# Kernel tuning notes

Hardware: AMD Instinct MI355X
Metric: run time of the kernel (lower is better)

The kernel has to match this reference:

```python
import jax, jax.numpy as jnp
import numpy as np

NUM_USERS = 1024
NUM_BUSINESSES = 2048
N_NODES = NUM_USERS + NUM_BUSINESSES  # 3072
B = 1024            # batch size (== NUM_USERS to keep the business_idx-offset bug valid)
E = 16384           # edges (self loops added inside reference, PyG GATConv default)
H = 768             # hidden_size
HEADS = 8
NUM_IMAGES = 3


def setup_inputs() -> dict:
    key = jax.random.key(0)
    ks = jax.random.split(key, 24)
    def rn(k, shape, s=0.02):
        return jax.random.normal(k, shape, dtype=jnp.float32) * s
    inp = {
        'text_cls': rn(ks[0], (B, 768), 1.0),              # BERT CLS features
        'img_cls': rn(ks[1], (B, NUM_IMAGES, 768), 1.0),   # ViT CLS features per image
        'biz_feats': rn(ks[2], (B, 3), 1.0),
        'W_text': rn(ks[3], (768, H)), 'b_text': jnp.zeros((H,), jnp.float32),
        'W_img': rn(ks[4], (768, H)), 'b_img': jnp.zeros((H,), jnp.float32),
        'W_bf': rn(ks[5], (3, H)), 'b_bf': jnp.zeros((H,), jnp.float32),
        'user_table': rn(ks[6], (NUM_USERS, H)),
        'biz_table': rn(ks[7], (NUM_BUSINESSES, H)),
        'W1': rn(ks[8], (H, HEADS * H)),
        'att_src1': rn(ks[9], (HEADS, H), 0.1),
        'att_dst1': rn(ks[10], (HEADS, H), 0.1),
        'b1': jnp.zeros((HEADS * H,), jnp.float32),
        'W2': rn(ks[11], (HEADS * H, H)),
        'att_src2': rn(ks[12], (1, H), 0.1),
        'att_dst2': rn(ks[13], (1, H), 0.1),
        'b2': jnp.zeros((H,), jnp.float32),
        'Wf1': rn(ks[14], (4 * H, 2 * H)), 'bf1': jnp.zeros((2 * H,), jnp.float32),
        'Wf2': rn(ks[15], (2 * H, H)), 'bf2': jnp.zeros((H,), jnp.float32),
        'Wf3': rn(ks[16], (H, 1)), 'bf3': jnp.zeros((1,), jnp.float32),
        'user_idx': jax.random.randint(ks[17], (B,), 0, NUM_USERS),
        'business_idx': jax.random.randint(ks[18], (B,), NUM_USERS, N_NODES),
        'edge_index': jax.random.randint(ks[19], (2, E), 0, N_NODES),
    }
    return inp


def gat_conv(x, src, dst, W, a_src, a_dst, bias, heads):
    # PyG GATConv: linear -> per-head additive attention -> scatter softmax over dst -> scatter add
    N = x.shape[0]
    C = W.shape[1] // heads
    h = (x @ W).reshape(N, heads, C)                       # [N,H,C]
    s_src = jnp.sum(h * a_src, axis=-1)                    # [N,H]
    s_dst = jnp.sum(h * a_dst, axis=-1)                    # [N,H]
    e = jax.nn.leaky_relu(s_src[src] + s_dst[dst], 0.2)    # [E,H]
    e_max = jax.ops.segment_max(e, dst, num_segments=N)    # [N,H]
    ee = jnp.exp(e - e_max[dst])
    denom = jax.ops.segment_sum(ee, dst, num_segments=N)   # [N,H]
    alpha = ee / (denom[dst] + 1e-16)                      # [E,H]
    out = jax.ops.segment_sum(h[src] * alpha[..., None], dst, num_segments=N)  # [N,H,C]
    return out.reshape(N, heads * C) + bias


def reference(text_cls, img_cls, biz_feats, W_text, b_text, W_img, b_img, W_bf, b_bf,
              user_table, biz_table, W1, att_src1, att_dst1, b1, W2, att_src2, att_dst2, b2,
              Wf1, bf1, Wf2, bf2, Wf3, bf3, user_idx, business_idx, edge_index):
    text_emb = text_cls @ W_text + b_text                       # TextEncoder.fc
    img_emb = jnp.mean(img_cls, axis=1) @ W_img + b_img         # ImageEncoder mean + fc
    meta = biz_feats @ W_bf + b_bf                              # business_feature_fc
    user_emb = user_table[user_idx]
    biz_emb = biz_table[business_idx - user_idx.shape[0]]       # faithful: offset by batch size
    x = jnp.zeros((N_NODES, H), jnp.float32)
    x = x.at[user_idx].set(user_emb)
    x = x.at[business_idx].set((text_emb + img_emb + meta + biz_emb) / 4.0)
    loop = jnp.arange(N_NODES)
    src = jnp.concatenate([edge_index[0], loop])                # add self loops (PyG default)
    dst = jnp.concatenate([edge_index[1], loop])
    x = jax.nn.relu(gat_conv(x, src, dst, W1, att_src1, att_dst1, b1, HEADS))
    x = gat_conv(x, src, dst, W2, att_src2, att_dst2, b2, 1)
    cat = jnp.concatenate([x[user_idx], x[business_idx], text_emb, img_emb], axis=1)  # [B,4H]
    h1 = jax.nn.relu(cat @ Wf1 + bf1)
    h2 = jax.nn.relu(h1 @ Wf2 + bf2)
    return (h2 @ Wf3 + bf3).squeeze(-1)                         # [B]
```

## Files before the change

kernel.cpp:

```cpp
#include <hip/hip_runtime.h>
#include <hip/hip_bf16.h>

namespace {

constexpr int kB = 1024;
constexpr int kNU = 1024;
constexpr int kNB = 2048;
constexpr int kNN = 3072;
constexpr int kE = 16384;
constexpr int kET = kE + kNN;
constexpr int kH = 768;
constexpr int kHeads = 8;
constexpr int kSplitK = 4;

typedef __attribute__((ext_vector_type(8))) short bf16x8_t;
typedef __attribute__((ext_vector_type(4))) float f32x4_t;

__device__ __forceinline__ float tof(float x) { return x; }
__device__ __forceinline__ float tof(__hip_bfloat16 x) { return __bfloat162float(x); }
__device__ __forceinline__ void stor(float* p, float v) { *p = v; }
__device__ __forceinline__ void stor(__hip_bfloat16* p, float v) { *p = __float2bfloat16(v); }

__device__ __forceinline__ float blo(unsigned u) {
  union { unsigned u; float f; } c; c.u = u << 16; return c.f;
}
__device__ __forceinline__ float bhi(unsigned u) {
  union { unsigned u; float f; } c; c.u = u & 0xffff0000u; return c.f;
}

__device__ __forceinline__ unsigned pk2(float a, float b) {
  union { __hip_bfloat16 h[2]; unsigned u; } c;
  c.h[0] = __float2bfloat16(a); c.h[1] = __float2bfloat16(b);
  return c.u;
}

__device__ __forceinline__ void gload_lds16(const void* g, void* l) {
  __builtin_amdgcn_global_load_lds(
      (const __attribute__((address_space(1))) void*)g,
      (__attribute__((address_space(3))) void*)l, 16, 0, 0);
}

template <int BM, int BN, int FM, int FN, typename TC>
__device__ __forceinline__ void gemm_body(
    const __hip_bfloat16* __restrict__ A, const __hip_bfloat16* __restrict__ Bt,
    const float* __restrict__ bias, TC* __restrict__ C,
    int K, int lda, int ldc, int act, int bx, int by) {
  __shared__ __align__(16) __hip_bfloat16 As[2][BM][32];
  __shared__ __align__(16) __hip_bfloat16 Bs[2][BN][32];
  const int t = threadIdx.x;
  const int w = t >> 6, lane = t & 63;
  const int wm = w >> 1, wn = w & 1;
  const int bm = by * BM, bn = bx * BN;
  const int lr = lane & 15, lg = lane >> 4;

  f32x4_t acc[FM][FN];
#pragma unroll
  for (int m = 0; m < FM; ++m)
#pragma unroll
    for (int n = 0; n < FN; ++n) acc[m][n] = (f32x4_t){0.f, 0.f, 0.f, 0.f};

  auto stage = [&](int buf, int kt) {
    const int k0 = kt << 5;
#pragma unroll
    for (int i = 0; i < BM / 64; ++i) {
      int L = i * 256 + t;
      gload_lds16(A + (size_t)(bm + (L >> 2)) * lda + k0 + (L & 3) * 8,
                  (char*)(&As[buf][0][0]) + ((size_t)(i * 256 + w * 64)) * 16);
    }
#pragma unroll
    for (int i = 0; i < BN / 64; ++i) {
      int L = i * 256 + t;
      gload_lds16(Bt + (size_t)(bn + (L >> 2)) * K + k0 + (L & 3) * 8,
                  (char*)(&Bs[buf][0][0]) + ((size_t)(i * 256 + w * 64)) * 16);
    }
  };

  const int NT = K >> 5;
  stage(0, 0);
  __syncthreads();
  for (int kt = 0; kt < NT; ++kt) {
    const int cur = kt & 1;
    if (kt + 1 < NT) stage(cur ^ 1, kt + 1);
    bf16x8_t af[FM], bv[FN];
#pragma unroll
    for (int m = 0; m < FM; ++m)
      af[m] = *(const bf16x8_t*)&As[cur][wm * FM * 16 + m * 16 + lr][lg * 8];
#pragma unroll
    for (int n = 0; n < FN; ++n)
      bv[n] = *(const bf16x8_t*)&Bs[cur][wn * FN * 16 + n * 16 + lr][lg * 8];
#pragma unroll
    for (int m = 0; m < FM; ++m)
#pragma unroll
      for (int n = 0; n < FN; ++n)
        acc[m][n] = __builtin_amdgcn_mfma_f32_16x16x32_bf16(af[m], bv[n], acc[m][n], 0, 0, 0);
    __syncthreads();
  }

#pragma unroll
  for (int m = 0; m < FM; ++m) {
    const int row0 = bm + wm * FM * 16 + m * 16 + lg * 4;
#pragma unroll
    for (int n = 0; n < FN; ++n) {
      const int cn = bn + wn * FN * 16 + n * 16 + lr;
      const float bvv = bias ? bias[cn] : 0.f;
#pragma unroll
      for (int r = 0; r < 4; ++r) {
        float v = acc[m][n][r] + bvv;
        if (act) v = fmaxf(v, 0.f);
        stor(&C[(size_t)(row0 + r) * ldc + cn], v);
      }
    }
  }
}

__device__ __forceinline__ void swz_xy(bool mfast, int& bx, int& by) {
  const int nwg = gridDim.x * gridDim.y;
  const int orig = blockIdx.y * gridDim.x + blockIdx.x;
  const int swz = (orig & 7) * (nwg >> 3) + (orig >> 3);
  if (mfast) { by = swz % gridDim.y; bx = swz / gridDim.y; }
  else       { bx = swz % gridDim.x; by = swz / gridDim.x; }
}

template <int BM, int BN, int FM, int FN, typename TC, bool MFAST>
__global__ __launch_bounds__(256) void mfma_gemm(
    const __hip_bfloat16* __restrict__ A, const __hip_bfloat16* __restrict__ Bt,
    const float* __restrict__ bias, TC* __restrict__ C,
    int N, int K, int act) {
  int bx, by;
  swz_xy(MFAST, bx, by);
  gemm_body<BM, BN, FM, FN, TC>(A, Bt, bias, C, K, K, N, act, bx, by);
}

template <int BM, int BN, int FM, int FN>
__global__ __launch_bounds__(256) void mfma_gemm_dual(
    const __hip_bfloat16* __restrict__ A0, const __hip_bfloat16* __restrict__ Bt0,
    const float* __restrict__ bias0, float* __restrict__ C0,
    const __hip_bfloat16* __restrict__ A1, const __hip_bfloat16* __restrict__ Bt1,
    const float* __restrict__ bias1, float* __restrict__ C1,
    int N, int K) {
  int bx, by;
  swz_xy(true, bx, by);
  const __hip_bfloat16* A = blockIdx.z ? A1 : A0;
  const __hip_bfloat16* Bt = blockIdx.z ? Bt1 : Bt0;
  const float* bias = blockIdx.z ? bias1 : bias0;
  float* C = blockIdx.z ? C1 : C0;
  gemm_body<BM, BN, FM, FN, float>(A, Bt, bias, C, K, K, N, 0, bx, by);
}

template <int BM, int BN, int FM, int FN>
__global__ __launch_bounds__(256) void gemm_head(
    const __hip_bfloat16* __restrict__ y, const __hip_bfloat16* __restrict__ W1t,
    const float* __restrict__ b1, __hip_bfloat16* __restrict__ x2) {
  const int hd = blockIdx.x;
  const int tile = blockIdx.y;
  const int bx = tile % (kH / BN);
  const int by = tile / (kH / BN);
  gemm_body<BM, BN, FM, FN, __hip_bfloat16>(
      y + (size_t)hd * kH, W1t + (size_t)hd * kH * kH, b1 + hd * kH,
      x2 + (size_t)hd * kH, kH, kHeads * kH, kHeads * kH, 1, bx, by);
}

template <int BM, int BN, int FM, int FN>
__global__ __launch_bounds__(256) void mfma_gemm_splitk(
    const __hip_bfloat16* __restrict__ A, const __hip_bfloat16* __restrict__ Bt,
    float* __restrict__ Cpart, int M, int N, int K, int KC) {
  __shared__ __align__(16) __hip_bfloat16 As[2][BM][32];
  __shared__ __align__(16) __hip_bfloat16 Bs[2][BN][32];
  int bx, by;
  swz_xy(false, bx, by);
  const int t = threadIdx.x;
  const int w = t >> 6, lane = t & 63;
  const int wm = w >> 1, wn = w & 1;
  const int bm = by * BM, bn = bx * BN;
  const int kbeg = blockIdx.z * KC;
  const int lr = lane & 15, lg = lane >> 4;

  f32x4_t acc[FM][FN];
#pragma unroll
  for (int m = 0; m < FM; ++m)
#pragma unroll
    for (int n = 0; n < FN; ++n) acc[m][n] = (f32x4_t){0.f, 0.f, 0.f, 0.f};

  auto stage = [&](int buf, int kt) {
    const int k0 = kbeg + (kt << 5);
#pragma unroll
    for (int i = 0; i < BM / 64; ++i) {
      int L = i * 256 + t;
      gload_lds16(A + (size_t)(bm + (L >> 2)) * K + k0 + (L & 3) * 8,
                  (char*)(&As[buf][0][0]) + ((size_t)(i * 256 + w * 64)) * 16);
    }
#pragma unroll
    for (int i = 0; i < BN / 64; ++i) {
      int L = i * 256 + t;
      gload_lds16(Bt + (size_t)(bn + (L >> 2)) * K + k0 + (L & 3) * 8,
                  (char*)(&Bs[buf][0][0]) + ((size_t)(i * 256 + w * 64)) * 16);
    }
  };

  const int NT = KC >> 5;
  stage(0, 0);
  __syncthreads();
  for (int kt = 0; kt < NT; ++kt) {
    const int cur = kt & 1;
    if (kt + 1 < NT) stage(cur ^ 1, kt + 1);
    bf16x8_t af[FM], bv[FN];
#pragma unroll
    for (int m = 0; m < FM; ++m)
      af[m] = *(const bf16x8_t*)&As[cur][wm * FM * 16 + m * 16 + lr][lg * 8];
#pragma unroll
    for (int n = 0; n < FN; ++n)
      bv[n] = *(const bf16x8_t*)&Bs[cur][wn * FN * 16 + n * 16 + lr][lg * 8];
#pragma unroll
    for (int m = 0; m < FM; ++m)
#pragma unroll
      for (int n = 0; n < FN; ++n)
        acc[m][n] = __builtin_amdgcn_mfma_f32_16x16x32_bf16(af[m], bv[n], acc[m][n], 0, 0, 0);
    __syncthreads();
  }

  float* Cp = Cpart + (size_t)blockIdx.z * M * N;
#pragma unroll
  for (int m = 0; m < FM; ++m) {
    const int row0 = bm + wm * FM * 16 + m * 16 + lg * 4;
#pragma unroll
    for (int n = 0; n < FN; ++n) {
      const int cn = bn + wn * FN * 16 + n * 16 + lr;
#pragma unroll
      for (int r = 0; r < 4; ++r) Cp[(size_t)(row0 + r) * N + cn] = acc[m][n][r];
    }
  }
}

__global__ __launch_bounds__(192) void reduce_scores2_kernel(
    const float* __restrict__ part, const float* __restrict__ att_src,
    const float* __restrict__ att_dst, __hip_bfloat16* __restrict__ h2,
    float* __restrict__ s_src, float* __restrict__ s_dst) {
  __shared__ float redS[3], redD[3];
  const int row = blockIdx.x;
  const int t = threadIdx.x;
  const int c = t * 4;
  const float* p = part + (size_t)row * kH + c;
  float4 s = *(const float4*)p;
#pragma unroll
  for (int z = 1; z < kSplitK; ++z) {
    float4 qv = *(const float4*)(p + (size_t)z * kNN * kH);
    s.x += qv.x; s.y += qv.y; s.z += qv.z; s.w += qv.w;
  }
  __hip_bfloat16 b0 = __float2bfloat16(s.x), b1 = __float2bfloat16(s.y);
  __hip_bfloat16 b2 = __float2bfloat16(s.z), b3 = __float2bfloat16(s.w);
  __hip_bfloat16* o = h2 + (size_t)row * kH + c;
  o[0] = b0; o[1] = b1; o[2] = b2; o[3] = b3;
  float f0 = tof(b0), f1 = tof(b1), f2 = tof(b2), f3 = tof(b3);
  float ss = f0 * att_src[c] + f1 * att_src[c + 1] + f2 * att_src[c + 2] + f3 * att_src[c + 3];
  float sd = f0 * att_dst[c] + f1 * att_dst[c + 1] + f2 * att_dst[c + 2] + f3 * att_dst[c + 3];
#pragma unroll
  for (int off = 32; off; off >>= 1) { ss += __shfl_down(ss, off); sd += __shfl_down(sd, off); }
  if ((t & 63) == 0) { redS[t >> 6] = ss; redD[t >> 6] = sd; }
  __syncthreads();
  if (t == 0) {
    s_src[row] = redS[0] + redS[1] + redS[2];
    s_dst[row] = redD[0] + redD[1] + redD[2];
  }
}

__global__ void reduce_relu_kernel(const float* __restrict__ part,
                                   const float* __restrict__ bias,
                                   __hip_bfloat16* __restrict__ outb, int MN4, int N) {
  int i = blockIdx.x * 256 + threadIdx.x;
  if (i >= MN4) return;
  float4 s = ((const float4*)part)[i];
  float4 p = ((const float4*)part)[(size_t)MN4 + i];
  int c = (i * 4) % N;
  float v0 = fmaxf(s.x + p.x + bias[c], 0.f);
  float v1 = fmaxf(s.y + p.y + bias[c + 1], 0.f);
  float v2 = fmaxf(s.z + p.z + bias[c + 2], 0.f);
  float v3 = fmaxf(s.w + p.w + bias[c + 3], 0.f);
  uint2 o;
  o.x = pk2(v0, v1); o.y = pk2(v2, v3);
  *(uint2*)(outb + (size_t)i * 4) = o;
}

__global__ __launch_bounds__(192) void reduce_final_kernel(
    const float* __restrict__ part, const float* __restrict__ bias,
    const float* __restrict__ Wf3, const float* __restrict__ bf3,
    float* __restrict__ out) {
  __shared__ float red[3];
  const int row = blockIdx.x;
  const int t = threadIdx.x;
  const int c = t * 4;
  const float* p0 = part + (size_t)row * kH + c;
  const float* p1 = p0 + (size_t)kB * kH;
  float4 a = *(const float4*)p0;
  float4 b = *(const float4*)p1;
  float v0 = fmaxf(a.x + b.x + bias[c], 0.f);
  float v1 = fmaxf(a.y + b.y + bias[c + 1], 0.f);
  float v2 = fmaxf(a.z + b.z + bias[c + 2], 0.f);
  float v3 = fmaxf(a.w + b.w + bias[c + 3], 0.f);
  float s = v0 * Wf3[c] + v1 * Wf3[c + 1] + v2 * Wf3[c + 2] + v3 * Wf3[c + 3];
#pragma unroll
  for (int off = 32; off; off >>= 1) s += __shfl_down(s, off);
  if ((t & 63) == 0) red[t >> 6] = s;
  __syncthreads();
  if (t == 0) out[row] = red[0] + red[1] + red[2] + bf3[0];
}

struct TJobs {
  const float* in[6];
  __hip_bfloat16* out[6];
  int K[6];
  int N[6];
  int start[7];
};

__global__ __launch_bounds__(256) void transp_prep_kernel(
    TJobs j, const float* __restrict__ text_cls, const float* __restrict__ img_cls,
    __hip_bfloat16* __restrict__ text_bf, __hip_bfloat16* __restrict__ imgm_bf,
    int prep_blocks, const float* __restrict__ W1, const float* __restrict__ a_src,
    const float* __restrict__ a_dst, float* __restrict__ wa) {
  __shared__ float tl[32][33];
  const int bid = blockIdx.x;
  const int t = threadIdx.x;
  if (bid >= j.start[6] + prep_blocks) {
    int gw = ((bid - j.start[6] - prep_blocks) * 256 + t) >> 6;
    int lane = t & 63;
    if (gw >= kHeads * kH) return;
    int i = gw >> 3, hd = gw & 7;
    const float* wrow = W1 + (size_t)i * (kHeads * kH) + hd * kH;
    const float* as = a_src + (size_t)hd * kH;
    const float* ad = a_dst + (size_t)hd * kH;
    float ss = 0.f, sd = 0.f;
    for (int c = lane; c < kH; c += 64) {
      float wv = wrow[c];
      ss = fmaf(wv, as[c], ss);
      sd = fmaf(wv, ad[c], sd);
    }
#pragma unroll
    for (int o = 32; o; o >>= 1) { ss += __shfl_down(ss, o); sd += __shfl_down(sd, o); }
    if (lane == 0) {
      wa[hd * kH + i] = ss;
      wa[kHeads * kH + hd * kH + i] = sd;
    }
    return;
  }
  if (bid >= j.start[6]) {
    int idx = (bid - j.start[6]) * 256 + t;
    if (idx < kB * kH) {
      text_bf[idx] = __float2bfloat16(text_cls[idx]);
      int b = idx / kH, c = idx - b * kH;
      const float* p = img_cls + (size_t)b * 3 * kH + c;
      imgm_bf[idx] = __float2bfloat16((p[0] + p[kH] + p[2 * kH]) * (1.f / 3.f));
    }
    return;
  }
  int idx = 0;
#pragma unroll
  for (int q = 1; q < 6; ++q)
    if (bid >= j.start[q]) idx = q;
  const int tile = bid - j.start[idx];
  const int N = j.N[idx], K = j.K[idx];
  const int tilesN = N >> 5;
  const int n0 = (tile % tilesN) << 5, k0 = (tile / tilesN) << 5;
  const float* in = j.in[idx];
  __hip_bfloat16* out = j.out[idx];
  const int r = t >> 3, c = (t & 7) * 4;
#pragma unroll
  for (int i = 0; i < 4; ++i) tl[r][c + i] = in[(size_t)(k0 + r) * N + n0 + c + i];
  __syncthreads();
  __hip_bfloat16* op = out + (size_t)(n0 + r) * K + k0 + c;
#pragma unroll
  for (int i = 0; i < 4; ++i) op[i] = __float2bfloat16(tl[c + i][r]);
}

__global__ __launch_bounds__(256) void s1_kernel(const __hip_bfloat16* __restrict__ xb,
                                                 const float* __restrict__ wa,
                                                 float* __restrict__ s1s,
                                                 float* __restrict__ s1d) {
  __shared__ unsigned xrow[kH / 2];
  const int n = blockIdx.x;
  const int t = threadIdx.x;
  const unsigned* xp = (const unsigned*)(xb + (size_t)n * kH);
  if (t < 128) { xrow[t] = xp[t]; xrow[t + 128] = xp[t + 128]; xrow[t + 256] = xp[t + 256]; }
  __syncthreads();
  const int w = t >> 6, lane = t & 63;
  const float* ws0 = wa + (size_t)w * kH;
  const float* wd0 = wa + (size_t)(kHeads + w) * kH;
  const float* ws1 = wa + (size_t)(w + 4) * kH;
  const float* wd1 = wa + (size_t)(kHeads + w + 4) * kH;
  float s0 = 0.f, d0 = 0.f, s1 = 0.f, d1 = 0.f;
  for (int u = lane; u < kH / 2; u += 64) {
    unsigned v = xrow[u];
    float f0 = blo(v), f1 = bhi(v);
    int c = u * 2;
    s0 = fmaf(f0, ws0[c], fmaf(f1, ws0[c + 1], s0));
    d0 = fmaf(f0, wd0[c], fmaf(f1, wd0[c + 1], d0));
    s1 = fmaf(f0, ws1[c], fmaf(f1, ws1[c + 1], s1));
    d1 = fmaf(f0, wd1[c], fmaf(f1, wd1[c + 1], d1));
  }
#pragma unroll
  for (int o = 32; o; o >>= 1) {
    s0 += __shfl_down(s0, o); d0 += __shfl_down(d0, o);
    s1 += __shfl_down(s1, o); d1 += __shfl_down(d1, o);
  }
  if (lane == 0) {
    s1s[n * 8 + w] = s0;     s1d[n * 8 + w] = d0;
    s1s[n * 8 + w + 4] = s1; s1d[n * 8 + w + 4] = d1;
  }
}

__global__ __launch_bounds__(256) void agg1x_kernel(
    const int* __restrict__ rowptr, const int* __restrict__ cols,
    const float* __restrict__ s1s, const float* __restrict__ s1d,
    const __hip_bfloat16* __restrict__ xb, __hip_bfloat16* __restrict__ y) {
  __shared__ float mh[8], rdh[8], sdl[8];
  __shared__ float alph[128][9];
  const int n = blockIdx.x;
  const int t = threadIdx.x, w = t >> 6, lane = t & 63;
  const int beg = rowptr[n], end = rowptr[n + 1];
  if (t < 8) sdl[t] = s1d[n * 8 + t];
  __syncthreads();
#pragma unroll
  for (int p = 0; p < 2; ++p) {
    const int h = w + p * 4;
    const float sd = sdl[h];
    float m = -3.402823466e38f;
    for (int i = beg + lane; i < end; i += 64) {
      float e = s1s[(size_t)cols[i] * 8 + h] + sd;
      e = (e > 0.f) ? e : 0.2f * e;
      m = fmaxf(m, e);
    }
#pragma unroll
    for (int o = 32; o; o >>= 1) m = fmaxf(m, __shfl_xor(m, o));
    float ds = 0.f;
    for (int i = beg + lane; i < end; i += 64) {
      float e = s1s[(size_t)cols[i] * 8 + h] + sd;
      e = (e > 0.f) ? e : 0.2f * e;
      ds += expf(e - m);
    }
#pragma unroll
    for (int o = 32; o; o >>= 1) ds += __shfl_xor(ds, o);
    if (lane == 0) { mh[h] = m; rdh[h] = 1.f / (ds + 1e-16f); }
  }
  __syncthreads();

  float acc[8][4];
#pragma unroll
  for (int h = 0; h < 8; ++h)
#pragma unroll
    for (int q = 0; q < 4; ++q) acc[h][q] = 0.f;
  const int c0 = t * 4;

  for (int chunk = beg; chunk < end; chunk += 128) {
    const int cnt = min(128, end - chunk);
#pragma unroll
    for (int p = 0; p < 2; ++p) {
      const int h = w + p * 4;
      const float sd = sdl[h], m = mh[h], rd = rdh[h];
      for (int i = lane; i < cnt; i += 64) {
        float e = s1s[(size_t)cols[chunk + i] * 8 + h] + sd;
        e = (e > 0.f) ? e : 0.2f * e;
        alph[i][h] = expf(e - m) * rd;
      }
    }
    __syncthreads();
    if (t < 192) {
      for (int i = 0; i < cnt; ++i) {
        int src = cols[chunk + i];
        uint2 v = *(const uint2*)(xb + (size_t)src * kH + c0);
        float f0 = blo(v.x), f1 = bhi(v.x), f2 = blo(v.y), f3 = bhi(v.y);
#pragma unroll
        for (int h = 0; h < 8; ++h) {
          float a = alph[i][h];
          acc[h][0] = fmaf(a, f0, acc[h][0]);
          acc[h][1] = fmaf(a, f1, acc[h][1]);
          acc[h][2] = fmaf(a, f2, acc[h][2]);
          acc[h][3] = fmaf(a, f3, acc[h][3]);
        }
      }
    }
    __syncthreads();
  }
  if (t < 192) {
#pragma unroll
    for (int h = 0; h < 8; ++h) {
      uint2 o;
      o.x = pk2(acc[h][0], acc[h][1]);
      o.y = pk2(acc[h][2], acc[h][3]);
      *(uint2*)(y + ((size_t)n * 8 + h) * kH + c0) = o;
    }
  }
}

__global__ void init_kernel(uint4* __restrict__ xb4, int* __restrict__ deg,
                            int* __restrict__ winner) {
  int i = blockIdx.x * 256 + threadIdx.x;
  if (i < kNN * kH * 2 / 16) xb4[i] = (uint4){0u, 0u, 0u, 0u};
  if (i < kNN) deg[i] = 0;
  if (i < kNB) winner[i] = -1;
}

__global__ void deg_winner_kernel(const int* __restrict__ ei, int* __restrict__ deg,
                                  const int* __restrict__ business_idx,
                                  int* __restrict__ winner) {
  int e = blockIdx.x * 256 + threadIdx.x;
  if (e < kET) {
    int dst = (e < kE) ? ei[kE + e] : (e - kE);
    atomicAdd(&deg[dst], 1);
  }
  if (e < kB) atomicMax(&winner[business_idx[e] - kNU], e);
}

__global__ __launch_bounds__(1024) void scan_kernel(const int* __restrict__ deg,
                                                    int* __restrict__ rowptr,
                                                    int* __restrict__ cursor) {
  __shared__ int sums[1024];
  int t = threadIdx.x;
  int v0 = deg[t * 3], v1 = deg[t * 3 + 1], v2 = deg[t * 3 + 2];
  int s = v0 + v1 + v2;
  sums[t] = s;
  __syncthreads();
  for (int o = 1; o < 1024; o <<= 1) {
    int xv = (t >= o) ? sums[t - o] : 0;
    __syncthreads();
    sums[t] += xv;
    __syncthreads();
  }
  int excl = sums[t] - s;
  rowptr[t * 3] = excl;          cursor[t * 3] = excl;
  rowptr[t * 3 + 1] = excl + v0; cursor[t * 3 + 1] = excl + v0;
  rowptr[t * 3 + 2] = excl + v0 + v1; cursor[t * 3 + 2] = excl + v0 + v1;
  if (t == 1023) rowptr[kNN] = excl + s;
}

__global__ void fill_kernel(const int* __restrict__ ei, int* __restrict__ cursor,
                            int* __restrict__ cols) {
  int e = blockIdx.x * 256 + threadIdx.x;
  if (e >= kET) return;
  int src, dst;
  if (e < kE) { src = ei[e]; dst = ei[kE + e]; } else { src = dst = e - kE; }
  int pos = atomicAdd(&cursor[dst], 1);
  cols[pos] = src;
}

__global__ void build_x_kernel(const int* __restrict__ user_idx,
                               const float* __restrict__ user_table,
                               const int* __restrict__ winner,
                               const float* __restrict__ text_emb,
                               const float* __restrict__ img_emb,
                               const float* __restrict__ biz_feats,
                               const float* __restrict__ W_bf,
                               const float* __restrict__ b_bf,
                               const float* __restrict__ biz_table,
                               __hip_bfloat16* __restrict__ xb) {
  int b = blockIdx.x;
  if (b < kNU) {
    int node = user_idx[b];
    for (int c = threadIdx.x; c < kH; c += blockDim.x)
      xb[(size_t)node * kH + c] = __float2bfloat16(user_table[(size_t)node * kH + c]);
  } else {
    int m = b - kNU;
    int w = winner[m];
    if (w < 0) return;
    int node = kNU + m;
    float f0 = biz_feats[w * 3], f1 = biz_feats[w * 3 + 1], f2 = biz_feats[w * 3 + 2];
    for (int c = threadIdx.x; c < kH; c += blockDim.x) {
      float meta = f0 * W_bf[c] + f1 * W_bf[kH + c] + f2 * W_bf[2 * kH + c] + b_bf[c];
      float v = (text_emb[(size_t)w * kH + c] + img_emb[(size_t)w * kH + c] + meta +
                 biz_table[(size_t)m * kH + c]) * 0.25f;
      xb[(size_t)node * kH + c] = __float2bfloat16(v);
    }
  }
}

__global__ __launch_bounds__(256) void gat_agg_kernel(
    const int* __restrict__ rowptr, const int* __restrict__ cols,
    const float* __restrict__ s_src, const float* __restrict__ s_dst,
    const __hip_bfloat16* __restrict__ h, const float* __restrict__ bias,
    float* __restrict__ out_f, int total) {
  const int pair = blockIdx.x * 4 + (threadIdx.x >> 6);
  if (pair >= total) return;
  const int lane = threadIdx.x & 63;
  const int n = pair;
  const int beg = rowptr[n], end = rowptr[n + 1];
  const float sdv = s_dst[pair];

  float m = -3.402823466e38f;
  for (int i = beg + lane; i < end; i += 64) {
    float e = s_src[cols[i]] + sdv;
    e = (e > 0.f) ? e : 0.2f * e;
    m = fmaxf(m, e);
  }
#pragma unroll
  for (int o = 32; o; o >>= 1) m = fmaxf(m, __shfl_xor(m, o));

  float dsum = 0.f;
  for (int i = beg + lane; i < end; i += 64) {
    float e = s_src[cols[i]] + sdv;
    e = (e > 0.f) ? e : 0.2f * e;
    dsum += expf(e - m);
  }
#pragma unroll
  for (int o = 32; o; o >>= 1) dsum += __shfl_xor(dsum, o);
  const float rdsum = 1.f / (dsum + 1e-16f);

  float a[12];
#pragma unroll
  for (int q = 0; q < 12; ++q) a[q] = 0.f;
  const size_t hoff = (size_t)lane * 4;
  for (int i = beg; i < end; ++i) {
    int src = cols[i];
    float e = s_src[src] + sdv;
    e = (e > 0.f) ? e : 0.2f * e;
    float wgt = expf(e - m) * rdsum;
    const __hip_bfloat16* hp = h + (size_t)src * kH + hoff;
#pragma unroll
    for (int j = 0; j < 3; ++j) {
      uint2 v = *(const uint2*)(hp + j * 256);
      a[j * 4 + 0] = fmaf(wgt, blo(v.x), a[j * 4 + 0]);
      a[j * 4 + 1] = fmaf(wgt, bhi(v.x), a[j * 4 + 1]);
      a[j * 4 + 2] = fmaf(wgt, blo(v.y), a[j * 4 + 2]);
      a[j * 4 + 3] = fmaf(wgt, bhi(v.y), a[j * 4 + 3]);
    }
  }
  const size_t ob = (size_t)n * kH + hoff;
#pragma unroll
  for (int j = 0; j < 3; ++j) {
#pragma unroll
    for (int q = 0; q < 4; ++q)
      out_f[ob + j * 256 + q] = a[j * 4 + q] + bias[hoff + j * 256 + q];
  }
}

__global__ void cat_kernel(const float* __restrict__ xf, const float* __restrict__ text_emb,
                           const float* __restrict__ img_emb, const int* __restrict__ user_idx,
                           const int* __restrict__ business_idx, __hip_bfloat16* __restrict__ cat) {
  int b = blockIdx.x;
  int u = user_idx[b], z = business_idx[b];
  __hip_bfloat16* crow = cat + (size_t)b * 4 * kH;
  for (int c = threadIdx.x; c < kH; c += blockDim.x) {
    crow[c] = __float2bfloat16(xf[(size_t)u * kH + c]);
    crow[kH + c] = __float2bfloat16(xf[(size_t)z * kH + c]);
    crow[2 * kH + c] = __float2bfloat16(text_emb[(size_t)b * kH + c]);
    crow[3 * kH + c] = __float2bfloat16(img_emb[(size_t)b * kH + c]);
  }
}

}

extern "C" void kernel_launch(void* const* d_in, const int* in_sizes, int n_in,
                              void* d_out, int out_size, void* d_ws, size_t ws_size,
                              hipStream_t stream) {
  const float* text_cls = (const float*)d_in[0];
  const float* img_cls = (const float*)d_in[1];
  const float* biz_feats = (const float*)d_in[2];
  const float* W_text = (const float*)d_in[3];
  const float* b_text = (const float*)d_in[4];
  const float* W_img = (const float*)d_in[5];
  const float* b_img = (const float*)d_in[6];
  const float* W_bf = (const float*)d_in[7];
  const float* b_bf = (const float*)d_in[8];
  const float* user_table = (const float*)d_in[9];
  const float* biz_table = (const float*)d_in[10];
  const float* W1 = (const float*)d_in[11];
  const float* att_src1 = (const float*)d_in[12];
  const float* att_dst1 = (const float*)d_in[13];
  const float* b1 = (const float*)d_in[14];
  const float* W2 = (const float*)d_in[15];
  const float* att_src2 = (const float*)d_in[16];
  const float* att_dst2 = (const float*)d_in[17];
  const float* b2 = (const float*)d_in[18];
  const float* Wf1 = (const float*)d_in[19];
  const float* bf1 = (const float*)d_in[20];
  const float* Wf2 = (const float*)d_in[21];
  const float* bf2 = (const float*)d_in[22];
  const float* Wf3 = (const float*)d_in[23];
  const float* bf3 = (const float*)d_in[24];
  const int* user_idx = (const int*)d_in[25];
  const int* business_idx = (const int*)d_in[26];
  const int* edge_index = (const int*)d_in[27];
  float* out = (float*)d_out;
  (void)in_sizes; (void)n_in; (void)out_size; (void)ws_size;

  char* base = (char*)d_ws;
  size_t off = 0;
  auto alloc = [&](size_t bytes) -> void* {
    void* p = base + off;
    off = (off + bytes + 255) & ~(size_t)255;
    return p;
  };
  __hip_bfloat16* xb = (__hip_bfloat16*)alloc((size_t)kNN * kH * 2);
  __hip_bfloat16* text_bf = (__hip_bfloat16*)alloc((size_t)kB * kH * 2);
  __hip_bfloat16* imgm_bf = (__hip_bfloat16*)alloc((size_t)kB * kH * 2);
  float* text_emb = (float*)alloc((size_t)kB * kH * 4);
  float* img_emb = (float*)alloc((size_t)kB * kH * 4);
  __hip_bfloat16* Wtt = (__hip_bfloat16*)alloc((size_t)kH * kH * 2);
  __hip_bfloat16* Wit = (__hip_bfloat16*)alloc((size_t)kH * kH * 2);
  __hip_bfloat16* W1t = (__hip_bfloat16*)alloc((size_t)kHeads * kH * kH * 2);
  __hip_bfloat16* W2t = (__hip_bfloat16*)alloc((size_t)kH * kHeads * kH * 2);
  __hip_bfloat16* Wf1t = (__hip_bfloat16*)alloc((size_t)2 * kH * 4 * kH * 2);
  __hip_bfloat16* Wf2t = (__hip_bfloat16*)alloc((size_t)kH * 2 * kH * 2);
  float* wa = (float*)alloc((size_t)2 * kHeads * kH * 4);
  __hip_bfloat16* y = (__hip_bfloat16*)alloc((size_t)kNN * kHeads * kH * 2);
  __hip_bfloat16* x2 = (__hip_bfloat16*)alloc((size_t)kNN * kHeads * kH * 2);
  __hip_bfloat16* h2 = (__hip_bfloat16*)alloc((size_t)kNN * kH * 2);
  float* xf = (float*)alloc((size_t)kNN * kH * 4);
  float* s1s = (float*)alloc((size_t)kNN * kHeads * 4);
  float* s1d = (float*)alloc((size_t)kNN * kHeads * 4);
  float* s2s = (float*)alloc((size_t)kNN * 4);
  float* s2d = (float*)alloc((size_t)kNN * 4);
  __hip_bfloat16* catb = (__hip_bfloat16*)alloc((size_t)kB * 4 * kH * 2);
  __hip_bfloat16* m1 = (__hip_bfloat16*)alloc((size_t)kB * 2 * kH * 2);
  float* m2 = (float*)alloc((size_t)kB * kH * 4);
  int* deg = (int*)alloc((size_t)kNN * 4);
  int* rowptr = (int*)alloc((size_t)(kNN + 1) * 4);
  int* cursor = (int*)alloc((size_t)kNN * 4);
  int* cols = (int*)alloc((size_t)kET * 4);
  int* winner = (int*)alloc((size_t)kNB * 4);
  (void)m2;

  float* part = (float*)y;

  init_kernel<<<(kNN * kH * 2 / 16 + 255) / 256, 256, 0, stream>>>((uint4*)xb, deg, winner);

  TJobs tj;
  tj.in[0] = W_text; tj.out[0] = Wtt;  tj.K[0] = kH;          tj.N[0] = kH;
  tj.in[1] = W_img;  tj.out[1] = Wit;  tj.K[1] = kH;          tj.N[1] = kH;
  tj.in[2] = W1;     tj.out[2] = W1t;  tj.K[2] = kH;          tj.N[2] = kHeads * kH;
  tj.in[3] = W2;     tj.out[3] = W2t;  tj.K[3] = kHeads * kH; tj.N[3] = kH;
  tj.in[4] = Wf1;    tj.out[4] = Wf1t; tj.K[4] = 4 * kH;      tj.N[4] = 2 * kH;
  tj.in[5] = Wf2;    tj.out[5] = Wf2t; tj.K[5] = 2 * kH;      tj.N[5] = kH;
  tj.start[0] = 0;
  for (int q = 0; q < 6; ++q)
    tj.start[q + 1] = tj.start[q] + (tj.K[q] / 32) * (tj.N[q] / 32);
  const int prep_blocks = (kB * kH + 255) / 256;
  const int wa_blocks = (kHeads * kH) / 4;
  transp_prep_kernel<<<tj.start[6] + prep_blocks + wa_blocks, 256, 0, stream>>>(
      tj, text_cls, img_cls, text_bf, imgm_bf, prep_blocks, W1, att_src1, att_dst1, wa);

  mfma_gemm_dual<64, 128, 2, 4><<<dim3(kH / 128, kB / 64, 2), 256, 0, stream>>>(
      text_bf, Wtt, b_text, text_emb, imgm_bf, Wit, b_img, img_emb, kH, kH);

  deg_winner_kernel<<<(kET + 255) / 256, 256, 0, stream>>>(edge_index, deg, business_idx, winner);
  scan_kernel<<<1, 1024, 0, stream>>>(deg, rowptr, cursor);
  fill_kernel<<<(kET + 255) / 256, 256, 0, stream>>>(edge_index, cursor, cols);

  build_x_kernel<<<kNN, 256, 0, stream>>>(user_idx, user_table, winner, text_emb, img_emb,
                                          biz_feats, W_bf, b_bf, biz_table, xb);

  s1_kernel<<<kNN, 256, 0, stream>>>(xb, wa, s1s, s1d);
  agg1x_kernel<<<kNN, 256, 0, stream>>>(rowptr, cols, s1s, s1d, xb, y);
  gemm_head<128, 128, 4, 4><<<dim3(kHeads, (kNN / 128) * (kH / 128)), 256, 0, stream>>>(
      y, W1t, b1, x2);

  mfma_gemm_splitk<64, 128, 2, 4><<<dim3(kH / 128, kNN / 64, kSplitK), 256, 0, stream>>>(
      x2, W2t, part, kNN, kH, kHeads * kH, kHeads * kH / kSplitK);
  reduce_scores2_kernel<<<kNN, 192, 0, stream>>>(part, att_src2, att_dst2, h2, s2s, s2d);
  gat_agg_kernel<<<kNN / 4, 256, 0, stream>>>(rowptr, cols, s2s, s2d, h2, b2, xf, kNN);

  cat_kernel<<<kB, 256, 0, stream>>>(xf, text_emb, img_emb, user_idx, business_idx, catb);
  mfma_gemm_splitk<64, 128, 2, 4><<<dim3(2 * kH / 128, kB / 64, 2), 256, 0, stream>>>(
      catb, Wf1t, part, kB, 2 * kH, 4 * kH, 2 * kH);
  reduce_relu_kernel<<<(kB * 2 * kH / 4 + 255) / 256, 256, 0, stream>>>(
      part, bf1, m1, kB * 2 * kH / 4, 2 * kH);
  mfma_gemm_splitk<64, 128, 2, 4><<<dim3(kH / 128, kB / 64, 2), 256, 0, stream>>>(
      m1, Wf2t, part, kB, kH, 2 * kH, kH);
  reduce_final_kernel<<<kB, 192, 0, stream>>>(part, bf2, Wf3, bf3, out);
}
```

Measured before the change: 270.7 us.

## Use K-pinned split-K GEMM for layer-2 projection and fold init into prep

Replaces the layer-2 W2 projection GEMM with a new kernel that puts the split-K index on the fastest grid dimension. It uses larger 128x128 tiles and 8 K-splits instead of 4, so blocks sharing an output tile run together and the tile count per split drops. The partial-sum buffer now spans y plus a new adjacent allocation, which means xf, catb and m1 have to be moved into that extended region. The separate init kernel is merged into the transpose/prep launch as extra blocks, saving one launch. In exchange the reduce step reads twice as many partial slices, and the larger buffer raises memory traffic.

```diff
diff --git a/kernel.cpp b/kernel.cpp
--- a/kernel.cpp
+++ b/kernel.cpp
@@ -11,7 +11,7 @@
 constexpr int kET = kE + kNN;
 constexpr int kH = 768;
 constexpr int kHeads = 8;
-constexpr int kSplitK = 4;
+constexpr int kS2 = 8;
 
 typedef __attribute__((ext_vector_type(8))) short bf16x8_t;
 typedef __attribute__((ext_vector_type(4))) float f32x4_t;
@@ -119,16 +119,6 @@
   const int swz = (orig & 7) * (nwg >> 3) + (orig >> 3);
   if (mfast) { by = swz % gridDim.y; bx = swz / gridDim.y; }
   else       { bx = swz % gridDim.x; by = swz / gridDim.x; }
-}
-
-template <int BM, int BN, int FM, int FN, typename TC, bool MFAST>
-__global__ __launch_bounds__(256) void mfma_gemm(
-    const __hip_bfloat16* __restrict__ A, const __hip_bfloat16* __restrict__ Bt,
-    const float* __restrict__ bias, TC* __restrict__ C,
-    int N, int K, int act) {
-  int bx, by;
-  swz_xy(MFAST, bx, by);
-  gemm_body<BM, BN, FM, FN, TC>(A, Bt, bias, C, K, K, N, act, bx, by);
 }
 
 template <int BM, int BN, int FM, int FN>
@@ -160,6 +150,81 @@
       x2 + (size_t)hd * kH, kH, kHeads * kH, kHeads * kH, 1, bx, by);
 }
 
+template <int BM, int BN, int FM, int FN, int S>
+__global__ __launch_bounds__(256) void mfma_gemm_kpin(
+    const __hip_bfloat16* __restrict__ A, const __hip_bfloat16* __restrict__ Bt,
+    float* __restrict__ Cpart, int M, int N, int K) {
+  __shared__ __align__(16) __hip_bfloat16 As[2][BM][32];
+  __shared__ __align__(16) __hip_bfloat16 Bs[2][BN][32];
+  const int kc = blockIdx.x;
+  const int tile = blockIdx.y;
+  const int tilesN = N / BN;
+  const int bx = tile % tilesN;
+  const int by = tile / tilesN;
+  const int KC = K / S;
+  const int kbeg = kc * KC;
+  const int t = threadIdx.x;
+  const int w = t >> 6, lane = t & 63;
+  const int wm = w >> 1, wn = w & 1;
+  const int bm = by * BM, bn = bx * BN;
+  const int lr = lane & 15, lg = lane >> 4;
+
+  f32x4_t acc[FM][FN];
+#pragma unroll
+  for (int m = 0; m < FM; ++m)
+#pragma unroll
+    for (int n = 0; n < FN; ++n) acc[m][n] = (f32x4_t){0.f, 0.f, 0.f, 0.f};
+
+  auto stage = [&](int buf, int kt) {
+    const int k0 = kbeg + (kt << 5);
+#pragma unroll
+    for (int i = 0; i < BM / 64; ++i) {
+      int L = i * 256 + t;
+      gload_lds16(A + (size_t)(bm + (L >> 2)) * K + k0 + (L & 3) * 8,
+                  (char*)(&As[buf][0][0]) + ((size_t)(i * 256 + w * 64)) * 16);
+    }
+#pragma unroll
+    for (int i = 0; i < BN / 64; ++i) {
+      int L = i * 256 + t;
+      gload_lds16(Bt + (size_t)(bn + (L >> 2)) * K + k0 + (L & 3) * 8,
+                  (char*)(&Bs[buf][0][0]) + ((size_t)(i * 256 + w * 64)) * 16);
+    }
+  };
+
+  const int NT = KC >> 5;
+  stage(0, 0);
+  __syncthreads();
+  for (int kt = 0; kt < NT; ++kt) {
+    const int cur = kt & 1;
+    if (kt + 1 < NT) stage(cur ^ 1, kt + 1);
+    bf16x8_t af[FM], bv[FN];
+#pragma unroll
+    for (int m = 0; m < FM; ++m)
+      af[m] = *(const bf16x8_t*)&As[cur][wm * FM * 16 + m * 16 + lr][lg * 8];
+#pragma unroll
+    for (int n = 0; n < FN; ++n)
+      bv[n] = *(const bf16x8_t*)&Bs[cur][wn * FN * 16 + n * 16 + lr][lg * 8];
+#pragma unroll
+    for (int m = 0; m < FM; ++m)
+#pragma unroll
+      for (int n = 0; n < FN; ++n)
+        acc[m][n] = __builtin_amdgcn_mfma_f32_16x16x32_bf16(af[m], bv[n], acc[m][n], 0, 0, 0);
+    __syncthreads();
+  }
+
+  float* Cp = Cpart + (size_t)kc * M * N;
+#pragma unroll
+  for (int m = 0; m < FM; ++m) {
+    const int row0 = bm + wm * FM * 16 + m * 16 + lg * 4;
+#pragma unroll
+    for (int n = 0; n < FN; ++n) {
+      const int cn = bn + wn * FN * 16 + n * 16 + lr;
+#pragma unroll
+      for (int r = 0; r < 4; ++r) Cp[(size_t)(row0 + r) * N + cn] = acc[m][n][r];
+    }
+  }
+}
+
 template <int BM, int BN, int FM, int FN>
 __global__ __launch_bounds__(256) void mfma_gemm_splitk(
     const __hip_bfloat16* __restrict__ A, const __hip_bfloat16* __restrict__ Bt,
@@ -242,7 +307,7 @@
   const float* p = part + (size_t)row * kH + c;
   float4 s = *(const float4*)p;
 #pragma unroll
-  for (int z = 1; z < kSplitK; ++z) {
+  for (int z = 1; z < kS2; ++z) {
     float4 qv = *(const float4*)(p + (size_t)z * kNN * kH);
     s.x += qv.x; s.y += qv.y; s.z += qv.z; s.w += qv.w;
   }
@@ -316,10 +381,19 @@
     TJobs j, const float* __restrict__ text_cls, const float* __restrict__ img_cls,
     __hip_bfloat16* __restrict__ text_bf, __hip_bfloat16* __restrict__ imgm_bf,
     int prep_blocks, const float* __restrict__ W1, const float* __restrict__ a_src,
-    const float* __restrict__ a_dst, float* __restrict__ wa) {
+    const float* __restrict__ a_dst, float* __restrict__ wa,
+    int wa_blocks, uint4* __restrict__ xb4, int* __restrict__ deg,
+    int* __restrict__ winner) {
   __shared__ float tl[32][33];
   const int bid = blockIdx.x;
   const int t = threadIdx.x;
+  if (bid >= j.start[6] + prep_blocks + wa_blocks) {
+    int i = (bid - j.start[6] - prep_blocks - wa_blocks) * 256 + t;
+    if (i < kNN * kH * 2 / 16) xb4[i] = (uint4){0u, 0u, 0u, 0u};
+    if (i < kNN) deg[i] = 0;
+    if (i < kNB) winner[i] = -1;
+    return;
+  }
   if (bid >= j.start[6] + prep_blocks) {
     int gw = ((bid - j.start[6] - prep_blocks) * 256 + t) >> 6;
     int lane = t & 63;
@@ -488,14 +562,6 @@
       *(uint2*)(y + ((size_t)n * 8 + h) * kH + c0) = o;
     }
   }
-}
-
-__global__ void init_kernel(uint4* __restrict__ xb4, int* __restrict__ deg,
-                            int* __restrict__ winner) {
-  int i = blockIdx.x * 256 + threadIdx.x;
-  if (i < kNN * kH * 2 / 16) xb4[i] = (uint4){0u, 0u, 0u, 0u};
-  if (i < kNN) deg[i] = 0;
-  if (i < kNB) winner[i] = -1;
 }
 
 __global__ void deg_winner_kernel(const int* __restrict__ ei, int* __restrict__ deg,
@@ -700,26 +766,22 @@
   __hip_bfloat16* Wf2t = (__hip_bfloat16*)alloc((size_t)kH * 2 * kH * 2);
   float* wa = (float*)alloc((size_t)2 * kHeads * kH * 4);
   __hip_bfloat16* y = (__hip_bfloat16*)alloc((size_t)kNN * kHeads * kH * 2);
+  char* ext = (char*)alloc((size_t)kNN * kHeads * kH * 2);
+  float* part = (float*)y;
+  float* xf = (float*)ext;
+  __hip_bfloat16* catb = (__hip_bfloat16*)(ext + 9437184);
+  __hip_bfloat16* m1 = (__hip_bfloat16*)(ext + 9437184 + 6291456);
   __hip_bfloat16* x2 = (__hip_bfloat16*)alloc((size_t)kNN * kHeads * kH * 2);
   __hip_bfloat16* h2 = (__hip_bfloat16*)alloc((size_t)kNN * kH * 2);
-  float* xf = (float*)alloc((size_t)kNN * kH * 4);
   float* s1s = (float*)alloc((size_t)kNN * kHeads * 4);
   float* s1d = (float*)alloc((size_t)kNN * kHeads * 4);
   float* s2s = (float*)alloc((size_t)kNN * 4);
   float* s2d = (float*)alloc((size_t)kNN * 4);
-  __hip_bfloat16* catb = (__hip_bfloat16*)alloc((size_t)kB * 4 * kH * 2);
-  __hip_bfloat16* m1 = (__hip_bfloat16*)alloc((size_t)kB * 2 * kH * 2);
-  float* m2 = (float*)alloc((size_t)kB * kH * 4);
   int* deg = (int*)alloc((size_t)kNN * 4);
   int* rowptr = (int*)alloc((size_t)(kNN + 1) * 4);
   int* cursor = (int*)alloc((size_t)kNN * 4);
   int* cols = (int*)alloc((size_t)kET * 4);
   int* winner = (int*)alloc((size_t)kNB * 4);
-  (void)m2;
-
-  float* part = (float*)y;
-
-  init_kernel<<<(kNN * kH * 2 / 16 + 255) / 256, 256, 0, stream>>>((uint4*)xb, deg, winner);
 
   TJobs tj;
   tj.in[0] = W_text; tj.out[0] = Wtt;  tj.K[0] = kH;          tj.N[0] = kH;
@@ -733,8 +795,10 @@
     tj.start[q + 1] = tj.start[q] + (tj.K[q] / 32) * (tj.N[q] / 32);
   const int prep_blocks = (kB * kH + 255) / 256;
   const int wa_blocks = (kHeads * kH) / 4;
-  transp_prep_kernel<<<tj.start[6] + prep_blocks + wa_blocks, 256, 0, stream>>>(
-      tj, text_cls, img_cls, text_bf, imgm_bf, prep_blocks, W1, att_src1, att_dst1, wa);
+  const int init_blocks = (kNN * kH * 2 / 16 + 255) / 256;
+  transp_prep_kernel<<<tj.start[6] + prep_blocks + wa_blocks + init_blocks, 256, 0, stream>>>(
+      tj, text_cls, img_cls, text_bf, imgm_bf, prep_blocks, W1, att_src1, att_dst1, wa,
+      wa_blocks, (uint4*)xb, deg, winner);
 
   mfma_gemm_dual<64, 128, 2, 4><<<dim3(kH / 128, kB / 64, 2), 256, 0, stream>>>(
       text_bf, Wtt, b_text, text_emb, imgm_bf, Wit, b_img, img_emb, kH, kH);
@@ -751,17 +815,18 @@
   gemm_head<128, 128, 4, 4><<<dim3(kHeads, (kNN / 128) * (kH / 128)), 256, 0, stream>>>(
       y, W1t, b1, x2);
 
-  mfma_gemm_splitk<64, 128, 2, 4><<<dim3(kH / 128, kNN / 64, kSplitK), 256, 0, stream>>>(
-      x2, W2t, part, kNN, kH, kHeads * kH, kHeads * kH / kSplitK);
+  mfma_gemm_kpin<128, 128, 4, 4, kS2>
+      <<<dim3(kS2, (kNN / 128) * (kH / 128)), 256, 0, stream>>>(
+          x2, W2t, part, kNN, kH, kHeads * kH);
   reduce_scores2_kernel<<<kNN, 192, 0, stream>>>(part, att_src2, att_dst2, h2, s2s, s2d);
   gat_agg_kernel<<<kNN / 4, 256, 0, stream>>>(rowptr, cols, s2s, s2d, h2, b2, xf, kNN);
 
   cat_kernel<<<kB, 256, 0, stream>>>(xf, text_emb, img_emb, user_idx, business_idx, catb);
   mfma_gemm_splitk<64, 128, 2, 4><<<dim3(2 * kH / 128, kB / 64, 2), 256, 0, stream>>>(
-      catb, Wf1t, part, kB, 2 * kH, 4 * kH, 2 * kH);
+      catb, Wf1t, (float*)y, kB, 2 * kH, 4 * kH, 2 * kH);
   reduce_relu_kernel<<<(kB * 2 * kH / 4 + 255) / 256, 256, 0, stream>>>(
-      part, bf1, m1, kB * 2 * kH / 4, 2 * kH);
+      (float*)y, bf1, m1, kB * 2 * kH / 4, 2 * kH);
   mfma_gemm_splitk<64, 128, 2, 4><<<dim3(kH / 128, kB / 64, 2), 256, 0, stream>>>(
-      m1, Wf2t, part, kB, kH, 2 * kH, kH);
-  reduce_final_kernel<<<kB, 192, 0, stream>>>(part, bf2, Wf3, bf3, out);
-}
+      m1, Wf2t, (float*)y, kB, kH, 2 * kH, kH);
+  reduce_final_kernel<<<kB, 192, 0, stream>>>((float*)y, bf2, Wf3, bf3, out);
+}
```

Measured after the change: 263.6 us. 2.6% less time.
